# Kernel tuning notes

Hardware: AMD Instinct MI355X
Metric: run time of the kernel (lower is better)

The kernel has to match this reference:

```python
import jax, jax.numpy as jnp
import numpy as np

D_MODEL, D_FF, N_EXPERTS, TOP_K = 1024, 4096, 8, 2

def setup_inputs() -> dict:
    key = jax.random.key(0)
    k0, k1, k2, k3 = jax.random.split(key, 4)
    x = jax.random.normal(k0, (2, 2048, D_MODEL), dtype=jnp.float32)
    Wg = jax.random.normal(k1, (D_MODEL, N_EXPERTS), dtype=jnp.float32) * 0.02
    W1 = jax.random.normal(k2, (N_EXPERTS, D_MODEL, D_FF), dtype=jnp.float32) * 0.02
    b1 = jnp.zeros((N_EXPERTS, D_FF), dtype=jnp.float32)
    W2 = jax.random.normal(k3, (N_EXPERTS, D_FF, D_MODEL), dtype=jnp.float32) * 0.02
    b2 = jnp.zeros((N_EXPERTS, D_MODEL), dtype=jnp.float32)
    return {"x": x, "Wg": Wg, "W1": W1, "b1": b1, "W2": W2, "b2": b2}

def reference(x, Wg, W1, b1, W2, b2):
    B = x.shape[:-1]
    xs = x.reshape(-1, x.shape[-1])                 # [T, D]
    T = xs.shape[0]
    gate_logits = xs @ Wg                           # [T, E]
    weights, sel = jax.lax.top_k(gate_logits, TOP_K)  # [T, k]
    # softmax over the top-k logits, computed in fp32 then cast back (matches F.softmax(dtype=float).type_as)
    weights = jax.nn.softmax(weights.astype(jnp.float32), axis=1).astype(x.dtype)
    # dense all-experts MLP: [E, T, D_FF] -> [E, T, D]
    h = jax.nn.relu(jnp.einsum('td,edf->etf', xs, W1) + b1[:, None, :])
    out_e = jnp.einsum('etf,efd->etd', h, W2) + b2[:, None, :]
    # gather each token's top-k expert outputs and combine with routing weights
    tok = jnp.arange(T)
    picked = out_e[sel, tok[:, None]]               # [T, k, D]
    out = jnp.einsum('tk,tkd->td', weights, picked) # [T, D]
    return out.reshape(*B, x.shape[-1])
```

## Files before the change

kernel.cpp:

```cpp
#include <hip/hip_runtime.h>
#include <cstdint>
#include <cstddef>

#define T_TOKENS 4096
#define DM 1024
#define DF 4096
#define NE 8
#define TOPK 2
#define BK 32
#define MAX_MT 72

typedef short short8 __attribute__((ext_vector_type(8)));
typedef float f32x4 __attribute__((ext_vector_type(4)));

__device__ __forceinline__ unsigned short f2h_bits(float f) {
  _Float16 h = (_Float16)f;
  union { _Float16 h; unsigned short u; } v; v.h = h; return v.u;
}

typedef __attribute__((address_space(3))) void lds_void_t;
typedef __attribute__((address_space(1))) void gvoid_t;
__device__ __forceinline__ void gl_lds16(const void* g, void* l) {
  __builtin_amdgcn_global_load_lds((gvoid_t*)g, (lds_void_t*)l, 16, 0, 0);
}

__global__ void gate_kernel(const float* __restrict__ x, const float* __restrict__ Wg,
                            int* __restrict__ sel, float* __restrict__ wts,
                            int* __restrict__ counts, unsigned short* __restrict__ Xh) {
  int wave = threadIdx.x >> 6, lane = threadIdx.x & 63;
  int t = blockIdx.x * 4 + wave;
  const float* xr = x + (size_t)t * DM;
  unsigned short* xh = Xh + (size_t)t * DM;
  float acc[NE];
#pragma unroll
  for (int e = 0; e < NE; e++) acc[e] = 0.f;
#pragma unroll
  for (int j = 0; j < DM / 64; j++) {
    int d = lane + 64 * j;
    float xv = xr[d];
    xh[d] = f2h_bits(xv);
    const float* wr = Wg + (size_t)d * NE;
#pragma unroll
    for (int e = 0; e < NE; e++) acc[e] += xv * wr[e];
  }
#pragma unroll
  for (int e = 0; e < NE; e++) {
    float v = acc[e];
#pragma unroll
    for (int off = 32; off > 0; off >>= 1) v += __shfl_down(v, off, 64);
    acc[e] = v;
  }
  if (lane == 0) {
    int b0 = 0;
#pragma unroll
    for (int e = 1; e < NE; e++) if (acc[e] > acc[b0]) b0 = e;
    int b1 = (b0 == 0) ? 1 : 0;
#pragma unroll
    for (int e = 0; e < NE; e++) if (e != b0 && acc[e] > acc[b1]) b1 = e;
    float p = expf(acc[b1] - acc[b0]);
    float w0 = 1.f / (1.f + p);
    sel[t * 2] = b0; sel[t * 2 + 1] = b1;
    wts[t * 2] = w0; wts[t * 2 + 1] = p * w0;
    atomicAdd(&counts[b0], 1);
    atomicAdd(&counts[b1], 1);
  }
}

__global__ void scan_kernel(const int* __restrict__ counts, int* __restrict__ offsets,
                            int* __restrict__ tile_off, int* __restrict__ cursors) {
  if (threadIdx.x == 0) {
    int o = 0, to = 0;
    offsets[0] = 0; tile_off[0] = 0;
    for (int e = 0; e < NE; e++) {
      cursors[e] = o;
      o += counts[e];
      to += (counts[e] + 127) >> 7;
      offsets[e + 1] = o;
      tile_off[e + 1] = to;
    }
  }
}

__global__ void scatter_kernel(const int* __restrict__ sel, const float* __restrict__ wts,
                               int* __restrict__ cursors, int* __restrict__ rows,
                               float* __restrict__ rw, int* __restrict__ inv) {
  int t = blockIdx.x * 256 + threadIdx.x;
  if (t >= T_TOKENS) return;
#pragma unroll
  for (int k = 0; k < TOPK; k++) {
    int e = sel[t * 2 + k];
    int slot = atomicAdd(&cursors[e], 1);
    rows[slot] = t;
    rw[slot] = wts[t * 2 + k];
    inv[t * 2 + k] = slot;
  }
}

__global__ void transpose_convert(const float* __restrict__ in, unsigned short* __restrict__ outp,
                                  int R, int C) {
  __shared__ unsigned short ldsT[64 * 72];
  const float* inE = in + (size_t)blockIdx.z * R * C;
  unsigned short* outE = outp + (size_t)blockIdx.z * R * C;
  int c0 = blockIdx.x * 64, r0 = blockIdx.y * 64;
  int tid = threadIdx.x;
  int rr = tid >> 4, cc4 = (tid & 15) * 4;
#pragma unroll
  for (int it = 0; it < 4; it++) {
    int r = rr + 16 * it;
    float4 v = *(const float4*)(inE + (size_t)(r0 + r) * C + c0 + cc4);
    ldsT[(cc4 + 0) * 72 + r] = f2h_bits(v.x);
    ldsT[(cc4 + 1) * 72 + r] = f2h_bits(v.y);
    ldsT[(cc4 + 2) * 72 + r] = f2h_bits(v.z);
    ldsT[(cc4 + 3) * 72 + r] = f2h_bits(v.w);
  }
  __syncthreads();
#pragma unroll
  for (int it = 0; it < 2; it++) {
    int idx = tid + 256 * it;
    int c = idx >> 3, r8 = (idx & 7) * 8;
    short8 val = *(const short8*)(ldsT + c * 72 + r8);
    *(short8*)(outE + (size_t)(c0 + c) * R + r0 + r8) = val;
  }
}

template <int K, int N, bool INDIR, bool SECOND>
__global__ __launch_bounds__(256, 2) void moe_gemm(
    const unsigned short* __restrict__ Aall, const unsigned short* __restrict__ Ball,
    unsigned short* __restrict__ Hout, float* __restrict__ Sout,
    const float* __restrict__ bias, const int* __restrict__ counts,
    const int* __restrict__ offsets, const int* __restrict__ tile_off,
    const int* __restrict__ rows, const float* __restrict__ rw) {
  __shared__ __align__(16) unsigned short lds[8704];
  unsigned short* ldsA = lds;
  unsigned short* ldsB = lds + 4096;

  int bx = blockIdx.x;
  int e = 0;
#pragma unroll 1
  while (e < NE && bx >= tile_off[e + 1]) e++;
  if (e >= NE) return;
  int lt = bx - tile_off[e];
  int cnt = counts[e];
  int m0 = lt * 128;
  int rowbase = offsets[e];
  int n0 = blockIdx.y * 128;

  const unsigned short* Be = Ball + ((size_t)e * N + n0) * K;

  int tid = threadIdx.x;
  int lane = tid & 63, wave = tid >> 6;
  int wm = wave & 1, wn = wave >> 1;

  int rA0 = tid >> 2, rA1 = (256 + tid) >> 2, seg = tid & 3;
  int mA0 = m0 + rA0; if (mA0 >= cnt) mA0 = cnt - 1;
  int mA1 = m0 + rA1; if (mA1 >= cnt) mA1 = cnt - 1;
  size_t ia0 = INDIR ? (size_t)rows[rowbase + mA0] : (size_t)(rowbase + mA0);
  size_t ia1 = INDIR ? (size_t)rows[rowbase + mA1] : (size_t)(rowbase + mA1);
  const unsigned short* srcA0 = Aall + ia0 * K + seg * 8;
  const unsigned short* srcA1 = Aall + ia1 * K + seg * 8;
  const unsigned short* srcB0 = Be + (size_t)rA0 * K + seg * 8;
  const unsigned short* srcB1 = Be + (size_t)rA1 * K + seg * 8;
  unsigned short* dA0 = ldsA + (size_t)tid * 8;
  unsigned short* dA1 = ldsA + (size_t)(256 + tid) * 8;
  unsigned short* dB0 = ldsB + (size_t)tid * 8;
  unsigned short* dB1 = ldsB + (size_t)(256 + tid) * 8;

  f32x4 acc[4][4] = {};

  for (int kk = 0; kk < K; kk += BK) {
    gl_lds16(srcA0 + kk, dA0);
    gl_lds16(srcA1 + kk, dA1);
    gl_lds16(srcB0 + kk, dB0);
    gl_lds16(srcB1 + kk, dB1);
    __syncthreads();

    short8 af[4], bfr[4];
#pragma unroll
    for (int t4 = 0; t4 < 4; t4++) {
      af[t4]  = *(const short8*)(ldsA + (wm * 64 + t4 * 16 + (lane & 15)) * BK + (lane >> 4) * 8);
      bfr[t4] = *(const short8*)(ldsB + (wn * 64 + t4 * 16 + (lane & 15)) * BK + (lane >> 4) * 8);
    }
#pragma unroll
    for (int tm = 0; tm < 4; tm++)
#pragma unroll
      for (int tn = 0; tn < 4; tn++)
        acc[tm][tn] = __builtin_amdgcn_mfma_f32_16x16x32_f16(af[tm], bfr[tn], acc[tm][tn], 0, 0, 0);
    __syncthreads();
  }

  int quad = lane >> 4, c16 = lane & 15;
  if constexpr (!SECOND) {
#pragma unroll 1
    for (int half = 0; half < 2; half++) {
      __syncthreads();
      if (wm == half) {
#pragma unroll
        for (int tm = 0; tm < 4; tm++) {
#pragma unroll
          for (int tn = 0; tn < 4; tn++) {
            int colL = wn * 64 + tn * 16 + c16;
            float b = bias[e * N + n0 + colL];
#pragma unroll
            for (int r = 0; r < 4; r++) {
              int rl = tm * 16 + quad * 4 + r;
              float v = fmaxf(acc[tm][tn][r] + b, 0.f);
              lds[rl * 136 + colL] = f2h_bits(v);
            }
          }
        }
      }
      __syncthreads();
#pragma unroll
      for (int i = 0; i < 4; i++) {
        int idx = tid + 256 * i;
        int row = idx >> 4, c8 = (idx & 15) * 8;
        int grow = m0 + half * 64 + row;
        if (grow < cnt) {
          short8 val = *(const short8*)(lds + row * 136 + c8);
          *(short8*)(Hout + (size_t)(rowbase + grow) * N + n0 + c8) = val;
        }
      }
    }
  } else {
#pragma unroll
    for (int tm = 0; tm < 4; tm++) {
#pragma unroll
      for (int tn = 0; tn < 4; tn++) {
        int gcol = n0 + wn * 64 + tn * 16 + c16;
        float b = bias[e * N + gcol];
#pragma unroll
        for (int r = 0; r < 4; r++) {
          int rl = wm * 64 + tm * 16 + quad * 4 + r;
          if (m0 + rl < cnt) {
            int slot = rowbase + m0 + rl;
            Sout[(size_t)slot * N + gcol] = (acc[tm][tn][r] + b) * rw[slot];
          }
        }
      }
    }
  }
}

__global__ void combine_kernel(const float* __restrict__ S, const int* __restrict__ inv,
                               float* __restrict__ out) {
  int wave = threadIdx.x >> 6, lane = threadIdx.x & 63;
  int t = blockIdx.x * 4 + wave;
  int s0 = inv[t * 2], s1 = inv[t * 2 + 1];
  const float4* a = (const float4*)(S + (size_t)s0 * DM);
  const float4* b = (const float4*)(S + (size_t)s1 * DM);
  float4* o = (float4*)(out + (size_t)t * DM);
#pragma unroll
  for (int j = 0; j < 4; j++) {
    float4 va = a[lane + 64 * j], vb = b[lane + 64 * j];
    float4 vo; vo.x = va.x + vb.x; vo.y = va.y + vb.y; vo.z = va.z + vb.z; vo.w = va.w + vb.w;
    o[lane + 64 * j] = vo;
  }
}

extern "C" void kernel_launch(void* const* d_in, const int* in_sizes, int n_in,
                              void* d_out, int out_size, void* d_ws, size_t ws_size,
                              hipStream_t stream) {
  const float* x  = (const float*)d_in[0];
  const float* Wg = (const float*)d_in[1];
  const float* W1 = (const float*)d_in[2];
  const float* b1 = (const float*)d_in[3];
  const float* W2 = (const float*)d_in[4];
  const float* b2 = (const float*)d_in[5];
  float* out = (float*)d_out;

  char* ws = (char*)d_ws;
  int*   counts   = (int*)(ws + 0);
  int*   cursors  = (int*)(ws + 64);
  int*   offsets  = (int*)(ws + 128);
  int*   tile_off = (int*)(ws + 192);
  int*   sel      = (int*)(ws + 256);
  float* wts      = (float*)(ws + 33024);
  int*   rows     = (int*)(ws + 65792);
  float* rw       = (float*)(ws + 98560);
  int*   inv      = (int*)(ws + 131328);
  unsigned short* Xh  = (unsigned short*)(ws + 164096);
  unsigned short* H   = (unsigned short*)(ws + 8552704);
  unsigned short* W1t = (unsigned short*)(ws + 75661568);
  float*          S   = (float*)(ws + 75661568);
  unsigned short* W2t = (unsigned short*)(ws + 142770432);

  hipMemsetAsync(ws, 0, 128, stream);

  gate_kernel<<<T_TOKENS / 4, 256, 0, stream>>>(x, Wg, sel, wts, counts, Xh);
  scan_kernel<<<1, 64, 0, stream>>>(counts, offsets, tile_off, cursors);
  scatter_kernel<<<T_TOKENS / 256, 256, 0, stream>>>(sel, wts, cursors, rows, rw, inv);
  transpose_convert<<<dim3(DF / 64, DM / 64, NE), 256, 0, stream>>>(W1, W1t, DM, DF);
  transpose_convert<<<dim3(DM / 64, DF / 64, NE), 256, 0, stream>>>(W2, W2t, DF, DM);

  moe_gemm<DM, DF, true, false><<<dim3(MAX_MT, DF / 128), 256, 0, stream>>>(
      Xh, W1t, H, nullptr, b1, counts, offsets, tile_off, rows, rw);
  moe_gemm<DF, DM, false, true><<<dim3(MAX_MT, DM / 128), 256, 0, stream>>>(
      H, W2t, nullptr, S, b2, counts, offsets, tile_off, rows, rw);

  combine_kernel<<<T_TOKENS / 4, 256, 0, stream>>>(S, inv, out);
}
```

Measured before the change: 713.6 us.

## Split-K the second expert GEMM and vectorize gate and transpose loads

The second GEMM (K=4096, N=1024) now splits its K dimension in two and doubles the grid, with each half writing partial sums into its own S buffer. The combine kernel then adds all four partials per token. The aim is to fill more compute units in a GEMM that otherwise launches only 8 column tiles per M tile. Separately, the gate kernel reads x as float4, and the transpose now stages fp32 in a padded LDS tile and converts on read. The cost is extra S traffic and twice the workspace for S, which must fit the existing layout.

```diff
diff --git a/kernel.cpp b/kernel.cpp
--- a/kernel.cpp
+++ b/kernel.cpp
@@ -9,6 +9,7 @@
 #define TOPK 2
 #define BK 32
 #define MAX_MT 72
+#define MSLOTS 8192
 
 typedef short short8 __attribute__((ext_vector_type(8)));
 typedef float f32x4 __attribute__((ext_vector_type(4)));
@@ -35,13 +36,21 @@
 #pragma unroll
   for (int e = 0; e < NE; e++) acc[e] = 0.f;
 #pragma unroll
-  for (int j = 0; j < DM / 64; j++) {
-    int d = lane + 64 * j;
-    float xv = xr[d];
-    xh[d] = f2h_bits(xv);
-    const float* wr = Wg + (size_t)d * NE;
-#pragma unroll
-    for (int e = 0; e < NE; e++) acc[e] += xv * wr[e];
+  for (int j = 0; j < 4; j++) {
+    int d4 = (lane + 64 * j) * 4;
+    float4 v = *(const float4*)(xr + d4);
+    ushort4 o;
+    o.x = f2h_bits(v.x); o.y = f2h_bits(v.y); o.z = f2h_bits(v.z); o.w = f2h_bits(v.w);
+    *(ushort4*)(xh + d4) = o;
+    const float* wr = Wg + (size_t)d4 * NE;
+#pragma unroll
+    for (int e = 0; e < NE; e++) acc[e] += v.x * wr[e];
+#pragma unroll
+    for (int e = 0; e < NE; e++) acc[e] += v.y * wr[NE + e];
+#pragma unroll
+    for (int e = 0; e < NE; e++) acc[e] += v.z * wr[2 * NE + e];
+#pragma unroll
+    for (int e = 0; e < NE; e++) acc[e] += v.w * wr[3 * NE + e];
   }
 #pragma unroll
   for (int e = 0; e < NE; e++) {
@@ -98,32 +107,34 @@
 
 __global__ void transpose_convert(const float* __restrict__ in, unsigned short* __restrict__ outp,
                                   int R, int C) {
-  __shared__ unsigned short ldsT[64 * 72];
+  __shared__ float tile[64 * 65];
   const float* inE = in + (size_t)blockIdx.z * R * C;
   unsigned short* outE = outp + (size_t)blockIdx.z * R * C;
   int c0 = blockIdx.x * 64, r0 = blockIdx.y * 64;
   int tid = threadIdx.x;
-  int rr = tid >> 4, cc4 = (tid & 15) * 4;
+  int rr = tid >> 4, c4 = (tid & 15) * 4;
 #pragma unroll
   for (int it = 0; it < 4; it++) {
     int r = rr + 16 * it;
-    float4 v = *(const float4*)(inE + (size_t)(r0 + r) * C + c0 + cc4);
-    ldsT[(cc4 + 0) * 72 + r] = f2h_bits(v.x);
-    ldsT[(cc4 + 1) * 72 + r] = f2h_bits(v.y);
-    ldsT[(cc4 + 2) * 72 + r] = f2h_bits(v.z);
-    ldsT[(cc4 + 3) * 72 + r] = f2h_bits(v.w);
+    float4 v = *(const float4*)(inE + (size_t)(r0 + r) * C + c0 + c4);
+    tile[r * 65 + c4 + 0] = v.x;
+    tile[r * 65 + c4 + 1] = v.y;
+    tile[r * 65 + c4 + 2] = v.z;
+    tile[r * 65 + c4 + 3] = v.w;
   }
   __syncthreads();
 #pragma unroll
   for (int it = 0; it < 2; it++) {
     int idx = tid + 256 * it;
     int c = idx >> 3, r8 = (idx & 7) * 8;
-    short8 val = *(const short8*)(ldsT + c * 72 + r8);
+    short8 val;
+#pragma unroll
+    for (int j = 0; j < 8; j++) val[j] = (short)f2h_bits(tile[(r8 + j) * 65 + c]);
     *(short8*)(outE + (size_t)(c0 + c) * R + r0 + r8) = val;
   }
 }
 
-template <int K, int N, bool INDIR, bool SECOND>
+template <int K, int N, bool INDIR, bool SECOND, int KSPLIT>
 __global__ __launch_bounds__(256, 2) void moe_gemm(
     const unsigned short* __restrict__ Aall, const unsigned short* __restrict__ Ball,
     unsigned short* __restrict__ Hout, float* __restrict__ Sout,
@@ -143,7 +154,10 @@
   int cnt = counts[e];
   int m0 = lt * 128;
   int rowbase = offsets[e];
-  int n0 = blockIdx.y * 128;
+  int nt = blockIdx.y % (N / 128);
+  int ks = blockIdx.y / (N / 128);
+  int n0 = nt * 128;
+  int k0 = ks * (K / KSPLIT);
 
   const unsigned short* Be = Ball + ((size_t)e * N + n0) * K;
 
@@ -167,7 +181,7 @@
 
   f32x4 acc[4][4] = {};
 
-  for (int kk = 0; kk < K; kk += BK) {
+  for (int kk = k0; kk < k0 + K / KSPLIT; kk += BK) {
     gl_lds16(srcA0 + kk, dA0);
     gl_lds16(srcA1 + kk, dA1);
     gl_lds16(srcB0 + kk, dB0);
@@ -222,18 +236,19 @@
       }
     }
   } else {
+    float* Sk = Sout + (size_t)ks * MSLOTS * N;
 #pragma unroll
     for (int tm = 0; tm < 4; tm++) {
 #pragma unroll
       for (int tn = 0; tn < 4; tn++) {
         int gcol = n0 + wn * 64 + tn * 16 + c16;
-        float b = bias[e * N + gcol];
+        float b = (ks == 0) ? bias[e * N + gcol] : 0.f;
 #pragma unroll
         for (int r = 0; r < 4; r++) {
           int rl = wm * 64 + tm * 16 + quad * 4 + r;
           if (m0 + rl < cnt) {
             int slot = rowbase + m0 + rl;
-            Sout[(size_t)slot * N + gcol] = (acc[tm][tn][r] + b) * rw[slot];
+            Sk[(size_t)slot * N + gcol] = (acc[tm][tn][r] + b) * rw[slot];
           }
         }
       }
@@ -246,14 +261,21 @@
   int wave = threadIdx.x >> 6, lane = threadIdx.x & 63;
   int t = blockIdx.x * 4 + wave;
   int s0 = inv[t * 2], s1 = inv[t * 2 + 1];
-  const float4* a = (const float4*)(S + (size_t)s0 * DM);
-  const float4* b = (const float4*)(S + (size_t)s1 * DM);
+  const float4* a0 = (const float4*)(S + (size_t)s0 * DM);
+  const float4* a1 = (const float4*)(S + (size_t)(MSLOTS + s0) * DM);
+  const float4* b0 = (const float4*)(S + (size_t)s1 * DM);
+  const float4* b1 = (const float4*)(S + (size_t)(MSLOTS + s1) * DM);
   float4* o = (float4*)(out + (size_t)t * DM);
 #pragma unroll
   for (int j = 0; j < 4; j++) {
-    float4 va = a[lane + 64 * j], vb = b[lane + 64 * j];
-    float4 vo; vo.x = va.x + vb.x; vo.y = va.y + vb.y; vo.z = va.z + vb.z; vo.w = va.w + vb.w;
-    o[lane + 64 * j] = vo;
+    int i = lane + 64 * j;
+    float4 va = a0[i], vb = a1[i], vc = b0[i], vd = b1[i];
+    float4 vo;
+    vo.x = (va.x + vb.x) + (vc.x + vd.x);
+    vo.y = (va.y + vb.y) + (vc.y + vd.y);
+    vo.z = (va.z + vb.z) + (vc.z + vd.z);
+    vo.w = (va.w + vb.w) + (vc.w + vd.w);
+    o[i] = vo;
   }
 }
 
@@ -292,9 +314,9 @@
   transpose_convert<<<dim3(DF / 64, DM / 64, NE), 256, 0, stream>>>(W1, W1t, DM, DF);
   transpose_convert<<<dim3(DM / 64, DF / 64, NE), 256, 0, stream>>>(W2, W2t, DF, DM);
 
-  moe_gemm<DM, DF, true, false><<<dim3(MAX_MT, DF / 128), 256, 0, stream>>>(
+  moe_gemm<DM, DF, true, false, 1><<<dim3(MAX_MT, DF / 128), 256, 0, stream>>>(
       Xh, W1t, H, nullptr, b1, counts, offsets, tile_off, rows, rw);
-  moe_gemm<DF, DM, false, true><<<dim3(MAX_MT, DM / 128), 256, 0, stream>>>(
+  moe_gemm<DF, DM, false, true, 2><<<dim3(MAX_MT, (DM / 128) * 2), 256, 0, stream>>>(
       H, W2t, nullptr, S, b2, counts, offsets, tile_off, rows, rw);
 
   combine_kernel<<<T_TOKENS / 4, 256, 0, stream>>>(S, inv, out);
```

After: 745.5 us. +4.5%, slower.
